# Performance work log

Hardware: AMD Instinct MI355X
Metric: run time of the kernel (lower is better)

The kernel has to match this reference:

```python
import jax, jax.numpy as jnp
import numpy as np
import math

EMBED_DIM = 256
NUM_HEADS = 8
FFN_DIM = 1024
EPS = 1e-5


def layer_norm(x, g, b):
    mu = jnp.mean(x, axis=-1, keepdims=True)
    var = jnp.var(x, axis=-1, keepdims=True)
    return (x - mu) / jnp.sqrt(var + EPS) * g + b


def setup_inputs() -> dict:
    key = jax.random.key(0)
    ks = jax.random.split(key, 10)
    B, L, D, F = 4, 2048, EMBED_DIM, FFN_DIM
    x = jax.random.normal(ks[0], (B, L, D), dtype=jnp.float32)
    mask = jnp.ones((B, L), dtype=jnp.int32)
    # FFN params (PyTorch Linear default-ish scale)
    W1 = jax.random.normal(ks[1], (D, F), dtype=jnp.float32) / np.sqrt(D)
    b1 = jnp.zeros((F,), dtype=jnp.float32)
    W2 = jax.random.normal(ks[2], (F, D), dtype=jnp.float32) / np.sqrt(F)
    b2 = jnp.zeros((D,), dtype=jnp.float32)
    g1 = jnp.ones((D,), dtype=jnp.float32)
    be1 = jnp.zeros((D,), dtype=jnp.float32)
    g2 = jnp.ones((D,), dtype=jnp.float32)
    be2 = jnp.zeros((D,), dtype=jnp.float32)
    return {"x": x, "mask": mask, "W1": W1, "b1": b1, "W2": W2, "b2": b2,
            "g1": g1, "be1": be1, "g2": g2, "be2": be2}


def quantum_attention(x, mask):
    B, L, D = x.shape
    H, dk = NUM_HEADS, D // NUM_HEADS
    xh = x.reshape(B, L, H, dk).transpose(0, 2, 1, 3)  # [B,H,L,dk]
    # per-token mean over batch and heads -> [L, dk]
    m = jnp.mean(xh, axis=(0, 1))
    # closed form of the single-qubit RX circuit: P(|1>) = sin^2(angle/2)
    dot = m @ m.T  # [L, L]
    ang = jnp.clip(dot, -math.pi, math.pi)
    scores = jnp.sin(ang * 0.5) ** 2  # [L, L], shared across B and H
    attn = jnp.broadcast_to(scores[None, None], (B, H, L, L))
    attn = jnp.where(mask[:, None, None, :] == 0, -1e9, attn)
    attn = jax.nn.softmax(attn, axis=-1)
    out = jnp.einsum('bhij,bhjd->bhid', attn, xh)  # values are xh itself
    return out.transpose(0, 2, 1, 3).reshape(B, L, D)


def reference(x, mask, W1, b1, W2, b2, g1, be1, g2, be2):
    attn_out = quantum_attention(x, mask)
    h = layer_norm(x + attn_out, g1, be1)
    ffn = jax.nn.relu(h @ W1 + b1) @ W2 + b2
    return layer_norm(h + ffn, g2, be2)
```

## Files before the change

### kernel.cpp

```cpp
#include <hip/hip_runtime.h>
#include <hip/hip_bf16.h>


#define B_ 4
#define L_ 2048
#define D_ 256
#define F_ 1024
#define PI_F 3.14159265358979323846f

typedef __bf16 bf16x8 __attribute__((ext_vector_type(8)));
typedef float floatx4 __attribute__((ext_vector_type(4)));
typedef unsigned short ushortx4 __attribute__((ext_vector_type(4)));

#define WAIT_VM(n) asm volatile("s_waitcnt vmcnt(" #n ")" ::: "memory")
#define SCHED0() __builtin_amdgcn_sched_barrier(0)
#define BARRIER() do { SCHED0(); __builtin_amdgcn_s_barrier(); SCHED0(); } while (0)

__device__ __forceinline__ unsigned short f2bf(float f) {
    unsigned int u = __float_as_uint(f);
    u = (u + 0x7FFFu + ((u >> 16) & 1u)) >> 16;
    return (unsigned short)u;
}
__device__ __forceinline__ float bf2f(unsigned short u) {
    union { unsigned int i; float f; } v; v.i = ((unsigned int)u) << 16; return v.f;
}

__device__ __forceinline__ void async_cp16(unsigned short* lds, const unsigned short* g) {
    __builtin_amdgcn_global_load_lds(
        (const __attribute__((address_space(1))) unsigned int*)g,
        (__attribute__((address_space(3))) unsigned int*)lds, 16, 0, 0);
}

__global__ __launch_bounds__(256) void k_prep(const float* __restrict__ x,
                                              const float* __restrict__ W1,
                                              const float* __restrict__ W2,
                                              const int* __restrict__ mask,
                                              unsigned short* __restrict__ mb,
                                              unsigned short* __restrict__ XmT,
                                              unsigned short* __restrict__ W1T,
                                              unsigned short* __restrict__ W2T) {
    __shared__ float tile[32][33];
    int r = blockIdx.x, t = threadIdx.x;
    if (r >= 2560) {
        if (r < 2816) {
            int idx = (r - 2560) * 256 + t;
            int l = idx >> 5, k = idx & 31;
            float s = 0.f;
#pragma unroll
            for (int b = 0; b < B_; b++) {
                const float* xp = x + ((size_t)(b * L_ + l)) * D_ + k;
#pragma unroll
                for (int h = 0; h < 8; h++) s += xp[h * 32];
            }
            mb[idx] = f2bf(s * (1.f / 32.f));
        } else {
#pragma unroll
            for (int c = 0; c < 32; c++) {
                int e = c * 256 + t;
                int b = e >> 11, j = e & (L_ - 1);
                XmT[(size_t)(1024 + b) * L_ + j] = mask[b * L_ + j] ? 0x3F80 : 0;
            }
        }
        return;
    }
    const float* in; unsigned short* outp; int R, C; const int* mrow = nullptr; size_t bo = 0;
    int bx, by;
    if (r < 2048) {
        int z = r >> 9, rem = r & 511; by = rem >> 3; bx = rem & 7;
        in = x; outp = XmT; R = L_; C = 256; bo = (size_t)z * R * C; mrow = mask + z * L_;
    } else if (r < 2304) {
        int rem = r - 2048; bx = rem & 31; by = rem >> 5;
        in = W1; outp = W1T; R = 256; C = 1024;
    } else {
        int rem = r - 2304; bx = rem & 7; by = rem >> 3;
        in = W2; outp = W2T; R = 1024; C = 256;
    }
    int r0 = by * 32, c0 = bx * 32;
    int tx = t & 31, ty = t >> 5;
#pragma unroll
    for (int rr = 0; rr < 4; rr++) {
        int rw = ty + rr * 8;
        tile[rw][tx] = in[bo + (size_t)(r0 + rw) * C + c0 + tx];
    }
    float mfac = 1.f;
    if (mrow) mfac = mrow[r0 + tx] ? 1.f : 0.f;
    __syncthreads();
#pragma unroll
    for (int rr = 0; rr < 4; rr++) {
        int c = ty + rr * 8;
        outp[bo + (size_t)(c0 + c) * R + r0 + tx] = f2bf(tile[tx][c] * mfac);
    }
}

__global__ __launch_bounds__(256) void k_scores_mfma(const unsigned short* __restrict__ mb,
                                                     unsigned short* __restrict__ E) {
    const int t = threadIdx.x, lane = t & 63, wid = t >> 6;
    const int wm = (wid >> 1) * 64, wn = (wid & 1) * 32;
    const int lr = lane & 15, lq = lane >> 4;
    int m0 = blockIdx.y * 128, n0 = blockIdx.x * 64;
    bf16x8 af[4], bfr[2];
#pragma unroll
    for (int i = 0; i < 4; i++)
        af[i] = *(const bf16x8*)(mb + (size_t)(m0 + wm + i * 16 + lr) * 32 + lq * 8);
#pragma unroll
    for (int j = 0; j < 2; j++)
        bfr[j] = *(const bf16x8*)(mb + (size_t)(n0 + wn + j * 16 + lr) * 32 + lq * 8);
    floatx4 acc[4][2];
#pragma unroll
    for (int i = 0; i < 4; i++)
#pragma unroll
        for (int j = 0; j < 2; j++) {
            acc[i][j] = (floatx4){0.f, 0.f, 0.f, 0.f};
            acc[i][j] = __builtin_amdgcn_mfma_f32_16x16x32_bf16(af[i], bfr[j], acc[i][j], 0, 0, 0);
        }
#pragma unroll
    for (int i = 0; i < 4; i++)
#pragma unroll
        for (int j = 0; j < 2; j++)
#pragma unroll
            for (int r = 0; r < 4; r++) {
                int row = m0 + wm + i * 16 + lq * 4 + r;
                int col = n0 + wn + j * 16 + lr;
                float d = fminf(fmaxf(acc[i][j][r], -PI_F), PI_F);
                float sn = __sinf(0.5f * d);
                E[(size_t)row * L_ + col] = f2bf(__expf(sn * sn));
            }
}

__global__ __launch_bounds__(256) void k_av(const unsigned short* __restrict__ E,
                                            const unsigned short* __restrict__ XmT,
                                            unsigned short* __restrict__ Cb) {
    __shared__ __align__(16) unsigned short sbuf[3][128 * 64 + 64 * 64];
    const int t = threadIdx.x, lane = t & 63, wid = t >> 6;
    const int wm = (wid >> 1) * 64, wn = (wid & 1) * 32;
    const int lr = lane & 15, lq = lane >> 4;
    const int lrow = lane >> 3, lseg = lane & 7;

    int bid = blockIdx.x;
    int swz = (bid & 7) * 34 + (bid >> 3);
    int m0 = (swz / 17) * 128, n0 = (swz % 17) * 64;

    const unsigned short* Ag[4]; int sAoff[4];
#pragma unroll
    for (int q = 0; q < 4; q++) {
        int rl = wid * 32 + q * 8 + lrow;
        Ag[q] = E + (size_t)(m0 + rl) * L_ + ((lseg - rl) & 7) * 8;
        sAoff[q] = (wid * 32 + q * 8) * 64;
    }
    const unsigned short* Bg[2]; int sBoff[2];
#pragma unroll
    for (int q = 0; q < 2; q++) {
        int rl = wid * 16 + q * 8 + lrow;
        Bg[q] = XmT + (size_t)(n0 + rl) * L_ + ((lseg - rl) & 7) * 8;
        sBoff[q] = 8192 + (wid * 16 + q * 8) * 64;
    }
    int arot[4], aroff[4], brot[2], broff[2];
#pragma unroll
    for (int i = 0; i < 4; i++) { int ar = wm + i * 16 + lr; aroff[i] = ar * 64; arot[i] = lq + ar; }
#pragma unroll
    for (int j = 0; j < 2; j++) { int br = wn + j * 16 + lr; broff[j] = 8192 + br * 64; brot[j] = lq + br; }

    floatx4 acc[4][2];
#pragma unroll
    for (int i = 0; i < 4; i++)
#pragma unroll
        for (int j = 0; j < 2; j++) acc[i][j] = (floatx4){0.f, 0.f, 0.f, 0.f};

    auto stage = [&](unsigned short* base, int k0) {
#pragma unroll
        for (int q = 0; q < 4; q++) async_cp16(base + sAoff[q], Ag[q] + k0);
#pragma unroll
        for (int q = 0; q < 2; q++) async_cp16(base + sBoff[q], Bg[q] + k0);
    };
    auto compute = [&](const unsigned short* base) {
#pragma unroll
        for (int s = 0; s < 2; s++) {
            bf16x8 af[4], bfr[2];
#pragma unroll
            for (int i = 0; i < 4; i++)
                af[i] = *(const bf16x8*)(base + aroff[i] + ((s * 4 + arot[i]) & 7) * 8);
#pragma unroll
            for (int j = 0; j < 2; j++)
                bfr[j] = *(const bf16x8*)(base + broff[j] + ((s * 4 + brot[j]) & 7) * 8);
#pragma unroll
            for (int i = 0; i < 4; i++)
#pragma unroll
                for (int j = 0; j < 2; j++)
                    acc[i][j] = __builtin_amdgcn_mfma_f32_16x16x32_bf16(af[i], bfr[j], acc[i][j], 0, 0, 0);
        }
    };

    unsigned short *p0 = sbuf[0], *p1 = sbuf[1], *p2 = sbuf[2];
    stage(p0, 0); stage(p1, 64); stage(p2, 128);
    WAIT_VM(12); BARRIER();
    for (int p = 0; p < 29; ++p) {
        compute(p0);
        BARRIER();
        stage(p0, (p + 3) << 6);
        WAIT_VM(12); BARRIER();
        unsigned short* tmp = p0; p0 = p1; p1 = p2; p2 = tmp;
    }
    compute(p0);
    BARRIER();
    WAIT_VM(6); BARRIER();
    compute(p1);
    BARRIER();
    WAIT_VM(0); BARRIER();
    compute(p2);

#pragma unroll
    for (int i = 0; i < 4; i++)
#pragma unroll
        for (int j = 0; j < 2; j++)
#pragma unroll
            for (int r = 0; r < 4; r++) {
                int row = m0 + wm + i * 16 + lq * 4 + r;
                int col = n0 + wn + j * 16 + lr;
                Cb[(size_t)row * 1088 + col] = f2bf(acc[i][j][r]);
            }
}

__global__ __launch_bounds__(256) void k_ln1(const float* __restrict__ x, const unsigned short* __restrict__ Cb,
                                             const float* __restrict__ g_, const float* __restrict__ be_,
                                             unsigned short* __restrict__ hb) {
    int t = threadIdx.x, wid = t >> 6, lane = t & 63;
    int tok = (blockIdx.x << 2) + wid;
    int b = tok >> 11, i = tok & (L_ - 1);
    float rs = bf2f(Cb[(size_t)i * 1088 + 1024 + b]);
    float4 xv = *(const float4*)(x + (size_t)tok * D_ + lane * 4);
    ushortx4 cv = *(const ushortx4*)(Cb + (size_t)i * 1088 + b * 256 + lane * 4);
    float v0 = xv.x + bf2f(cv.x) / rs;
    float v1 = xv.y + bf2f(cv.y) / rs;
    float v2 = xv.z + bf2f(cv.z) / rs;
    float v3 = xv.w + bf2f(cv.w) / rs;
    float s  = v0 + v1 + v2 + v3;
    float s2 = v0 * v0 + v1 * v1 + v2 * v2 + v3 * v3;
#pragma unroll
    for (int o = 1; o < 64; o <<= 1) { s += __shfl_xor(s, o); s2 += __shfl_xor(s2, o); }
    float mu = s * (1.f / 256.f);
    float var = s2 * (1.f / 256.f) - mu * mu;
    float r = rsqrtf(var + 1e-5f);
    float4 gv = *(const float4*)(g_ + lane * 4);
    float4 bv = *(const float4*)(be_ + lane * 4);
    ushortx4 o4;
    o4.x = f2bf((v0 - mu) * r * gv.x + bv.x);
    o4.y = f2bf((v1 - mu) * r * gv.y + bv.y);
    o4.z = f2bf((v2 - mu) * r * gv.z + bv.z);
    o4.w = f2bf((v3 - mu) * r * gv.w + bv.w);
    *(ushortx4*)(hb + (size_t)tok * D_ + lane * 4) = o4;
}

__global__ __launch_bounds__(256) void k_gemm1(const unsigned short* __restrict__ hb,
                                               const unsigned short* __restrict__ W1T,
                                               const float* __restrict__ b1, unsigned short* __restrict__ t1) {
    __shared__ __align__(16) unsigned short sbuf[2][128 * 64 + 128 * 64];
    const int t = threadIdx.x, lane = t & 63, wid = t >> 6;
    const int wm = (wid >> 1) * 64, wn = (wid & 1) * 64;
    const int lr = lane & 15, lq = lane >> 4;
    const int lrow8 = lane >> 3, lseg = lane & 7;

    int bid = blockIdx.x;
    int swz = (bid & 7) * 64 + (bid >> 3);
    int m0 = (swz >> 3) * 128, n0 = (swz & 7) * 128;

    const unsigned short* Ag[4]; const unsigned short* Bg[4]; int aoff[4], boff4[4];
#pragma unroll
    for (int q = 0; q < 4; q++) {
        int rl = q * 32 + wid * 8 + lrow8;
        int seg = (lseg - rl) & 7;
        Ag[q] = hb + (size_t)(m0 + rl) * 256 + seg * 8;
        Bg[q] = W1T + (size_t)(n0 + rl) * 256 + seg * 8;
        aoff[q] = (q * 32 + wid * 8) * 64;
        boff4[q] = 8192 + (q * 32 + wid * 8) * 64;
    }
    int arot[4], aroff[4], brot[4], broff[4];
#pragma unroll
    for (int i = 0; i < 4; i++) { int ar = wm + i * 16 + lr; aroff[i] = ar * 64; arot[i] = lq + ar; }
#pragma unroll
    for (int j = 0; j < 4; j++) { int br = wn + j * 16 + lr; broff[j] = 8192 + br * 64; brot[j] = lq + br; }

    floatx4 acc[4][4];
#pragma unroll
    for (int i = 0; i < 4; i++)
#pragma unroll
        for (int j = 0; j < 4; j++) acc[i][j] = (floatx4){0.f, 0.f, 0.f, 0.f};

    auto stage = [&](unsigned short* base, int k0) {
#pragma unroll
        for (int q = 0; q < 4; q++) { async_cp16(base + aoff[q], Ag[q] + k0); async_cp16(base + boff4[q], Bg[q] + k0); }
    };
    auto compute = [&](const unsigned short* base) {
#pragma unroll
        for (int s = 0; s < 2; s++) {
            bf16x8 af[4], bfr[4];
#pragma unroll
            for (int i = 0; i < 4; i++) af[i] = *(const bf16x8*)(base + aroff[i] + ((s * 4 + arot[i]) & 7) * 8);
#pragma unroll
            for (int j = 0; j < 4; j++) bfr[j] = *(const bf16x8*)(base + broff[j] + ((s * 4 + brot[j]) & 7) * 8);
#pragma unroll
            for (int i = 0; i < 4; i++)
#pragma unroll
                for (int j = 0; j < 4; j++)
                    acc[i][j] = __builtin_amdgcn_mfma_f32_16x16x32_bf16(af[i], bfr[j], acc[i][j], 0, 0, 0);
        }
    };

    unsigned short *pa = sbuf[0], *pb = sbuf[1];
    stage(pa, 0); stage(pb, 64);
    WAIT_VM(8); BARRIER();
    compute(pa);
    BARRIER();
    stage(pa, 128);
    WAIT_VM(8); BARRIER();
    compute(pb);
    BARRIER();
    stage(pb, 192);
    WAIT_VM(8); BARRIER();
    compute(pa);
    BARRIER();
    WAIT_VM(0); BARRIER();
    compute(pb);

    float bb[4];
#pragma unroll
    for (int j = 0; j < 4; j++) bb[j] = b1[n0 + wn + j * 16 + lr];
#pragma unroll
    for (int i = 0; i < 4; i++)
#pragma unroll
        for (int j = 0; j < 4; j++) {
            int col = n0 + wn + j * 16 + lr;
#pragma unroll
            for (int r = 0; r < 4; r++) {
                int row = m0 + wm + i * 16 + lq * 4 + r;
                t1[(size_t)row * 1024 + col] = f2bf(fmaxf(acc[i][j][r] + bb[j], 0.f));
            }
        }
}

__global__ __launch_bounds__(256) void k_gemm2ln(const unsigned short* __restrict__ t1,
                                                 const unsigned short* __restrict__ W2T,
                                                 const float* __restrict__ b2,
                                                 const unsigned short* __restrict__ hb,
                                                 const float* __restrict__ g_, const float* __restrict__ be_,
                                                 float* __restrict__ out) {
    __shared__ __align__(16) unsigned short sbuf[3][32 * 64 + 256 * 64];
    __shared__ float red[4][32][2];
    const int t = threadIdx.x, lane = t & 63, wid = t >> 6;
    const int wn = wid * 64;
    const int lr = lane & 15, lq = lane >> 4;
    const int lrow8 = lane >> 3, lseg = lane & 7;
    int m0 = blockIdx.x * 32;

    int arl = wid * 8 + lrow8;
    const unsigned short* Ag = t1 + (size_t)(m0 + arl) * 1024 + (((lseg - arl) & 7) * 8);
    int sAoff = (wid * 8) * 64;
    const unsigned short* Bg[8]; int sBoff[8];
#pragma unroll
    for (int q = 0; q < 8; q++) {
        int rl = q * 32 + wid * 8 + lrow8;
        Bg[q] = W2T + (size_t)rl * 1024 + (((lseg - rl) & 7) * 8);
        sBoff[q] = 2048 + (q * 32 + wid * 8) * 64;
    }
    int aroff[2], arot[2];
#pragma unroll
    for (int i = 0; i < 2; i++) { int ar = i * 16 + lr; aroff[i] = ar * 64; arot[i] = lq + ar; }
    int brot[4], broff[4];
#pragma unroll
    for (int j = 0; j < 4; j++) { int br = wn + j * 16 + lr; broff[j] = 2048 + br * 64; brot[j] = lq + br; }

    floatx4 acc[2][4];
#pragma unroll
    for (int i = 0; i < 2; i++)
#pragma unroll
        for (int j = 0; j < 4; j++) acc[i][j] = (floatx4){0.f, 0.f, 0.f, 0.f};

    auto stage = [&](unsigned short* base, int k0) {
        async_cp16(base + sAoff, Ag + k0);
#pragma unroll
        for (int q = 0; q < 8; q++) async_cp16(base + sBoff[q], Bg[q] + k0);
    };
    auto compute = [&](const unsigned short* base) {
#pragma unroll
        for (int s = 0; s < 2; s++) {
            bf16x8 af[2];
#pragma unroll
            for (int i = 0; i < 2; i++)
                af[i] = *(const bf16x8*)(base + aroff[i] + ((s * 4 + arot[i]) & 7) * 8);
#pragma unroll
            for (int j = 0; j < 4; j++) {
                bf16x8 bfr = *(const bf16x8*)(base + broff[j] + ((s * 4 + brot[j]) & 7) * 8);
#pragma unroll
                for (int i = 0; i < 2; i++)
                    acc[i][j] = __builtin_amdgcn_mfma_f32_16x16x32_bf16(af[i], bfr, acc[i][j], 0, 0, 0);
            }
        }
    };

    unsigned short *p0 = sbuf[0], *p1 = sbuf[1], *p2 = sbuf[2];
    stage(p0, 0); stage(p1, 64); stage(p2, 128);
    WAIT_VM(18); BARRIER();
    for (int p = 0; p < 13; ++p) {
        compute(p0);
        BARRIER();
        stage(p0, (p + 3) << 6);
        WAIT_VM(18); BARRIER();
        unsigned short* tmp = p0; p0 = p1; p1 = p2; p2 = tmp;
    }
    compute(p0);
    BARRIER();
    WAIT_VM(9); BARRIER();
    compute(p1);
    BARRIER();
    WAIT_VM(0); BARRIER();
    compute(p2);

    float psum[2][4], psq[2][4];
#pragma unroll
    for (int i = 0; i < 2; i++)
#pragma unroll
        for (int r = 0; r < 4; r++) { psum[i][r] = 0.f; psq[i][r] = 0.f; }
#pragma unroll
    for (int i = 0; i < 2; i++)
#pragma unroll
        for (int j = 0; j < 4; j++) {
            int col = wn + j * 16 + lr;
            float bv = b2[col];
#pragma unroll
            for (int r = 0; r < 4; r++) {
                int row = m0 + i * 16 + lq * 4 + r;
                float v = acc[i][j][r] + bv + bf2f(hb[(size_t)row * 256 + col]);
                acc[i][j][r] = v;
                psum[i][r] += v; psq[i][r] += v * v;
            }
        }
#pragma unroll
    for (int o = 1; o < 16; o <<= 1)
#pragma unroll
        for (int i = 0; i < 2; i++)
#pragma unroll
            for (int r = 0; r < 4; r++) { psum[i][r] += __shfl_xor(psum[i][r], o); psq[i][r] += __shfl_xor(psq[i][r], o); }
    if (lr == 0) {
#pragma unroll
        for (int i = 0; i < 2; i++)
#pragma unroll
            for (int r = 0; r < 4; r++) {
                int lrow = i * 16 + lq * 4 + r;
                red[wid][lrow][0] = psum[i][r];
                red[wid][lrow][1] = psq[i][r];
            }
    }
    __syncthreads();
#pragma unroll
    for (int i = 0; i < 2; i++)
#pragma unroll
        for (int r = 0; r < 4; r++) {
            int lrow = i * 16 + lq * 4 + r;
            float s  = red[0][lrow][0] + red[1][lrow][0] + red[2][lrow][0] + red[3][lrow][0];
            float s2 = red[0][lrow][1] + red[1][lrow][1] + red[2][lrow][1] + red[3][lrow][1];
            float mu = s * (1.f / 256.f);
            float var = s2 * (1.f / 256.f) - mu * mu;
            float rc = rsqrtf(var + 1e-5f);
            int row = m0 + lrow;
#pragma unroll
            for (int j = 0; j < 4; j++) {
                int col = wn + j * 16 + lr;
                out[(size_t)row * 256 + col] = (acc[i][j][r] - mu) * rc * g_[col] + be_[col];
            }
        }
}

extern "C" void kernel_launch(void* const* d_in, const int* in_sizes, int n_in,
                              void* d_out, int out_size, void* d_ws, size_t ws_size,
                              hipStream_t stream) {
    const float* x   = (const float*)d_in[0];
    const int*  mask = (const int*)d_in[1];
    const float* W1  = (const float*)d_in[2];
    const float* b1  = (const float*)d_in[3];
    const float* W2  = (const float*)d_in[4];
    const float* b2  = (const float*)d_in[5];
    const float* g1  = (const float*)d_in[6];
    const float* be1 = (const float*)d_in[7];
    const float* g2  = (const float*)d_in[8];
    const float* be2 = (const float*)d_in[9];
    float* out = (float*)d_out;

    char* w = (char*)d_ws;
    unsigned short* mb_   = (unsigned short*)w;  w += 65536 * 2;
    unsigned short* E_    = (unsigned short*)w;  w += (size_t)L_ * L_ * 2;
    unsigned short* XmT_  = (unsigned short*)w;  w += (size_t)1088 * L_ * 2;
    unsigned short* W1T_  = (unsigned short*)w;  w += 262144 * 2;
    unsigned short* W2T_  = (unsigned short*)w;  w += 262144 * 2;
    unsigned short* Cb_   = (unsigned short*)w;  w += (size_t)L_ * 1088 * 2;
    unsigned short* hb_   = (unsigned short*)w;  w += (size_t)8192 * 256 * 2;
    unsigned short* t1_   = (unsigned short*)w;  w += (size_t)8192 * 1024 * 2;

    k_prep<<<2817, 256, 0, stream>>>(x, W1, W2, mask, mb_, XmT_, W1T_, W2T_);
    k_scores_mfma<<<dim3(32, 16), 256, 0, stream>>>(mb_, E_);
    k_av<<<272, 256, 0, stream>>>(E_, XmT_, Cb_);
    k_ln1<<<2048, 256, 0, stream>>>(x, Cb_, g1, be1, hb_);
    k_gemm1<<<512, 256, 0, stream>>>(hb_, W1T_, b1, t1_);
    k_gemm2ln<<<256, 256, 0, stream>>>(t1_, W2T_, b2, hb_, g2, be2, out);
}
```

Baseline: 137.5 us.

## Fuse LN1, FFN GEMM1 and GEMM2+LN2 into a single streaming kernel

Replaces the three kernels (LN1, GEMM1, GEMM2+LN2) with one fused kernel. Each block of 32 tokens computes LN1 into LDS, then loops over 64-wide FFN chunks: GEMM1 chunk, bias+ReLU into an LDS tile, and an immediate GEMM2 accumulate. W1/W2 chunks are double-buffered with async loads, and the residual is read back from LDS. This removes the global round-trips of the hb and t1 intermediates and two launches. The cost is only 256 blocks at one block per CU, many barriers per chunk, and GEMM1 recomputed with small tiles, so latency hiding may suffer.

```diff
diff --git a/kernel.cpp b/kernel.cpp
--- a/kernel.cpp
+++ b/kernel.cpp
@@ -11,8 +11,10 @@
 typedef __bf16 bf16x8 __attribute__((ext_vector_type(8)));
 typedef float floatx4 __attribute__((ext_vector_type(4)));
 typedef unsigned short ushortx4 __attribute__((ext_vector_type(4)));
+typedef unsigned short ushortx8 __attribute__((ext_vector_type(8)));
 
 #define WAIT_VM(n) asm volatile("s_waitcnt vmcnt(" #n ")" ::: "memory")
+#define WAIT_LGKM() asm volatile("s_waitcnt lgkmcnt(0)" ::: "memory")
 #define SCHED0() __builtin_amdgcn_sched_barrier(0)
 #define BARRIER() do { SCHED0(); __builtin_amdgcn_s_barrier(); SCHED0(); } while (0)
 
@@ -220,215 +222,195 @@
             }
 }
 
-__global__ __launch_bounds__(256) void k_ln1(const float* __restrict__ x, const unsigned short* __restrict__ Cb,
-                                             const float* __restrict__ g_, const float* __restrict__ be_,
-                                             unsigned short* __restrict__ hb) {
-    int t = threadIdx.x, wid = t >> 6, lane = t & 63;
-    int tok = (blockIdx.x << 2) + wid;
-    int b = tok >> 11, i = tok & (L_ - 1);
-    float rs = bf2f(Cb[(size_t)i * 1088 + 1024 + b]);
-    float4 xv = *(const float4*)(x + (size_t)tok * D_ + lane * 4);
-    ushortx4 cv = *(const ushortx4*)(Cb + (size_t)i * 1088 + b * 256 + lane * 4);
-    float v0 = xv.x + bf2f(cv.x) / rs;
-    float v1 = xv.y + bf2f(cv.y) / rs;
-    float v2 = xv.z + bf2f(cv.z) / rs;
-    float v3 = xv.w + bf2f(cv.w) / rs;
-    float s  = v0 + v1 + v2 + v3;
-    float s2 = v0 * v0 + v1 * v1 + v2 * v2 + v3 * v3;
-#pragma unroll
-    for (int o = 1; o < 64; o <<= 1) { s += __shfl_xor(s, o); s2 += __shfl_xor(s2, o); }
-    float mu = s * (1.f / 256.f);
-    float var = s2 * (1.f / 256.f) - mu * mu;
-    float r = rsqrtf(var + 1e-5f);
-    float4 gv = *(const float4*)(g_ + lane * 4);
-    float4 bv = *(const float4*)(be_ + lane * 4);
-    ushortx4 o4;
-    o4.x = f2bf((v0 - mu) * r * gv.x + bv.x);
-    o4.y = f2bf((v1 - mu) * r * gv.y + bv.y);
-    o4.z = f2bf((v2 - mu) * r * gv.z + bv.z);
-    o4.w = f2bf((v3 - mu) * r * gv.w + bv.w);
-    *(ushortx4*)(hb + (size_t)tok * D_ + lane * 4) = o4;
-}
-
-__global__ __launch_bounds__(256) void k_gemm1(const unsigned short* __restrict__ hb,
-                                               const unsigned short* __restrict__ W1T,
-                                               const float* __restrict__ b1, unsigned short* __restrict__ t1) {
-    __shared__ __align__(16) unsigned short sbuf[2][128 * 64 + 128 * 64];
+__global__ __launch_bounds__(256, 1) void k_ffn(const float* __restrict__ x,
+                                                const unsigned short* __restrict__ Cb,
+                                                const unsigned short* __restrict__ W1T,
+                                                const unsigned short* __restrict__ W2T,
+                                                const float* __restrict__ b1,
+                                                const float* __restrict__ b2,
+                                                const float* __restrict__ g1, const float* __restrict__ be1,
+                                                const float* __restrict__ g2, const float* __restrict__ be2,
+                                                float* __restrict__ out) {
+    __shared__ __align__(16) unsigned short hA[4 * 32 * 64];
+    __shared__ __align__(16) unsigned short W1b[2][4 * 64 * 64];
+    __shared__ __align__(16) unsigned short W2b[4 * 64 * 64];
+    __shared__ __align__(16) unsigned short t1c[32 * 72];
+    __shared__ float red[4][32][2];
+
     const int t = threadIdx.x, lane = t & 63, wid = t >> 6;
-    const int wm = (wid >> 1) * 64, wn = (wid & 1) * 64;
     const int lr = lane & 15, lq = lane >> 4;
-    const int lrow8 = lane >> 3, lseg = lane & 7;
-
-    int bid = blockIdx.x;
-    int swz = (bid & 7) * 64 + (bid >> 3);
-    int m0 = (swz >> 3) * 128, n0 = (swz & 7) * 128;
-
-    const unsigned short* Ag[4]; const unsigned short* Bg[4]; int aoff[4], boff4[4];
-#pragma unroll
-    for (int q = 0; q < 4; q++) {
-        int rl = q * 32 + wid * 8 + lrow8;
-        int seg = (lseg - rl) & 7;
-        Ag[q] = hb + (size_t)(m0 + rl) * 256 + seg * 8;
-        Bg[q] = W1T + (size_t)(n0 + rl) * 256 + seg * 8;
-        aoff[q] = (q * 32 + wid * 8) * 64;
-        boff4[q] = 8192 + (q * 32 + wid * 8) * 64;
-    }
-    int arot[4], aroff[4], brot[4], broff[4];
-#pragma unroll
-    for (int i = 0; i < 4; i++) { int ar = wm + i * 16 + lr; aroff[i] = ar * 64; arot[i] = lq + ar; }
-#pragma unroll
-    for (int j = 0; j < 4; j++) { int br = wn + j * 16 + lr; broff[j] = 8192 + br * 64; brot[j] = lq + br; }
-
-    floatx4 acc[4][4];
-#pragma unroll
-    for (int i = 0; i < 4; i++)
+    const int half = lane >> 5, l32 = lane & 31;
+    const int m0 = blockIdx.x * 32;
+
+    float b1v[16];
+#pragma unroll
+    for (int c = 0; c < 16; c++) b1v[c] = b1[c * 64 + wid * 16 + lr];
+    float4 g1a = *(const float4*)(g1 + l32 * 8);
+    float4 g1b = *(const float4*)(g1 + l32 * 8 + 4);
+    float4 be1a = *(const float4*)(be1 + l32 * 8);
+    float4 be1b = *(const float4*)(be1 + l32 * 8 + 4);
+    WAIT_VM(0);
+
+    auto stageW1 = [&](unsigned short* buf, int fc) {
+#pragma unroll
+        for (int q = 0; q < 8; q++) {
+            int kc = q >> 1, sub = q & 1;
+            int fl = sub * 32 + wid * 8 + (lane >> 3);
+            int kk = lane & 7;
+            const unsigned short* src = W1T + (size_t)(fc * 64 + fl) * 256 + kc * 64 + (((kk - fl) & 7) * 8);
+            async_cp16(W1b[0] + (buf - W1b[0]) + kc * 4096 + sub * 2048 + wid * 512, src);
+        }
+    };
+    auto stageW2 = [&](int fc) {
+#pragma unroll
+        for (int q = 0; q < 8; q++) {
+            int nc = q >> 1, sub = q & 1;
+            int nl = sub * 32 + wid * 8 + (lane >> 3);
+            int kk = lane & 7;
+            const unsigned short* src = W2T + (size_t)(nc * 64 + nl) * 1024 + fc * 64 + (((kk - nl) & 7) * 8);
+            async_cp16(W2b + nc * 4096 + sub * 2048 + wid * 512, src);
+        }
+    };
+    stageW1(W1b[0], 0);
+    stageW2(0);
+    stageW1(W1b[1], 1);
+
+#pragma unroll
+    for (int it = 0; it < 4; it++) {
+        int tloc = wid * 8 + it * 2 + half;
+        int tok = m0 + tloc;
+        int bi = tok >> 11, ii = tok & (L_ - 1);
+        float rs = bf2f(Cb[(size_t)ii * 1088 + 1024 + bi]);
+        float4 xv0 = *(const float4*)(x + (size_t)tok * D_ + l32 * 8);
+        float4 xv1 = *(const float4*)(x + (size_t)tok * D_ + l32 * 8 + 4);
+        ushortx8 cv = *(const ushortx8*)(Cb + (size_t)ii * 1088 + bi * 256 + l32 * 8);
+        float v[8];
+        v[0] = xv0.x + bf2f(cv[0]) / rs; v[1] = xv0.y + bf2f(cv[1]) / rs;
+        v[2] = xv0.z + bf2f(cv[2]) / rs; v[3] = xv0.w + bf2f(cv[3]) / rs;
+        v[4] = xv1.x + bf2f(cv[4]) / rs; v[5] = xv1.y + bf2f(cv[5]) / rs;
+        v[6] = xv1.z + bf2f(cv[6]) / rs; v[7] = xv1.w + bf2f(cv[7]) / rs;
+        float s = 0.f, s2 = 0.f;
+#pragma unroll
+        for (int k = 0; k < 8; k++) { s += v[k]; s2 += v[k] * v[k]; }
+#pragma unroll
+        for (int o = 1; o < 32; o <<= 1) { s += __shfl_xor(s, o); s2 += __shfl_xor(s2, o); }
+        float mu = s * (1.f / 256.f);
+        float var = s2 * (1.f / 256.f) - mu * mu;
+        float rq = rsqrtf(var + 1e-5f);
+        union { bf16x8 v8; unsigned short u[8]; } hv;
+        hv.u[0] = f2bf((v[0] - mu) * rq * g1a.x + be1a.x);
+        hv.u[1] = f2bf((v[1] - mu) * rq * g1a.y + be1a.y);
+        hv.u[2] = f2bf((v[2] - mu) * rq * g1a.z + be1a.z);
+        hv.u[3] = f2bf((v[3] - mu) * rq * g1a.w + be1a.w);
+        hv.u[4] = f2bf((v[4] - mu) * rq * g1b.x + be1b.x);
+        hv.u[5] = f2bf((v[5] - mu) * rq * g1b.y + be1b.y);
+        hv.u[6] = f2bf((v[6] - mu) * rq * g1b.z + be1b.z);
+        hv.u[7] = f2bf((v[7] - mu) * rq * g1b.w + be1b.w);
+        *(bf16x8*)(hA + (l32 >> 3) * 2048 + tloc * 64 + ((((l32 & 7) + tloc) & 7) * 8)) = hv.v8;
+    }
+    WAIT_LGKM(); BARRIER();
+
+    bf16x8 haf[2][8];
+#pragma unroll
+    for (int i = 0; i < 2; i++)
+#pragma unroll
+        for (int kc = 0; kc < 4; kc++)
+#pragma unroll
+            for (int s = 0; s < 2; s++) {
+                int row = i * 16 + lr;
+                haf[i][kc * 2 + s] = *(const bf16x8*)(hA + kc * 2048 + row * 64 + (((s * 4 + lq + row) & 7) * 8));
+            }
+
+    floatx4 acc[2][4];
+#pragma unroll
+    for (int i = 0; i < 2; i++)
 #pragma unroll
         for (int j = 0; j < 4; j++) acc[i][j] = (floatx4){0.f, 0.f, 0.f, 0.f};
 
-    auto stage = [&](unsigned short* base, int k0) {
-#pragma unroll
-        for (int q = 0; q < 4; q++) { async_cp16(base + aoff[q], Ag[q] + k0); async_cp16(base + boff4[q], Bg[q] + k0); }
-    };
-    auto compute = [&](const unsigned short* base) {
+    const int wcol = wid * 16 + lr;
+    auto gemm1 = [&](const unsigned short* wb, floatx4 a1[2]) {
+#pragma unroll
+        for (int kc = 0; kc < 4; kc++)
+#pragma unroll
+            for (int s = 0; s < 2; s++) {
+                bf16x8 bfr = *(const bf16x8*)(wb + kc * 4096 + wcol * 64 + (((s * 4 + lq + wcol) & 7) * 8));
+                a1[0] = __builtin_amdgcn_mfma_f32_16x16x32_bf16(haf[0][kc * 2 + s], bfr, a1[0], 0, 0, 0);
+                a1[1] = __builtin_amdgcn_mfma_f32_16x16x32_bf16(haf[1][kc * 2 + s], bfr, a1[1], 0, 0, 0);
+            }
+    };
+    auto t1write = [&](floatx4 a1[2], float bv) {
+#pragma unroll
+        for (int i = 0; i < 2; i++)
+#pragma unroll
+            for (int r = 0; r < 4; r++)
+                t1c[(i * 16 + lq * 4 + r) * 72 + wcol] = f2bf(fmaxf(a1[i][r] + bv, 0.f));
+    };
+    auto gemm2 = [&]() {
 #pragma unroll
         for (int s = 0; s < 2; s++) {
-            bf16x8 af[4], bfr[4];
-#pragma unroll
-            for (int i = 0; i < 4; i++) af[i] = *(const bf16x8*)(base + aroff[i] + ((s * 4 + arot[i]) & 7) * 8);
-#pragma unroll
-            for (int j = 0; j < 4; j++) bfr[j] = *(const bf16x8*)(base + broff[j] + ((s * 4 + brot[j]) & 7) * 8);
-#pragma unroll
-            for (int i = 0; i < 4; i++)
-#pragma unroll
-                for (int j = 0; j < 4; j++)
-                    acc[i][j] = __builtin_amdgcn_mfma_f32_16x16x32_bf16(af[i], bfr[j], acc[i][j], 0, 0, 0);
-        }
-    };
-
-    unsigned short *pa = sbuf[0], *pb = sbuf[1];
-    stage(pa, 0); stage(pb, 64);
-    WAIT_VM(8); BARRIER();
-    compute(pa);
-    BARRIER();
-    stage(pa, 128);
-    WAIT_VM(8); BARRIER();
-    compute(pb);
-    BARRIER();
-    stage(pb, 192);
-    WAIT_VM(8); BARRIER();
-    compute(pa);
-    BARRIER();
-    WAIT_VM(0); BARRIER();
-    compute(pb);
-
-    float bb[4];
-#pragma unroll
-    for (int j = 0; j < 4; j++) bb[j] = b1[n0 + wn + j * 16 + lr];
-#pragma unroll
-    for (int i = 0; i < 4; i++)
+            bf16x8 af0 = *(const bf16x8*)(t1c + lr * 72 + s * 32 + lq * 8);
+            bf16x8 af1 = *(const bf16x8*)(t1c + (16 + lr) * 72 + s * 32 + lq * 8);
+#pragma unroll
+            for (int j = 0; j < 4; j++) {
+                int nl = j * 16 + lr;
+                bf16x8 bfr = *(const bf16x8*)(W2b + wid * 4096 + nl * 64 + (((s * 4 + lq + nl) & 7) * 8));
+                acc[0][j] = __builtin_amdgcn_mfma_f32_16x16x32_bf16(af0, bfr, acc[0][j], 0, 0, 0);
+                acc[1][j] = __builtin_amdgcn_mfma_f32_16x16x32_bf16(af1, bfr, acc[1][j], 0, 0, 0);
+            }
+        }
+    };
+
+#pragma unroll
+    for (int c = 0; c < 14; c++) {
+        floatx4 a1[2] = { (floatx4){0.f,0.f,0.f,0.f}, (floatx4){0.f,0.f,0.f,0.f} };
+        gemm1(W1b[c & 1], a1);
+        BARRIER();
+        stageW1(W1b[c & 1], c + 2);
+        t1write(a1, b1v[c]);
+        WAIT_LGKM();
+        WAIT_VM(8); BARRIER();
+        gemm2();
+        BARRIER();
+        stageW2(c + 1);
+    }
+    {
+        floatx4 a1[2] = { (floatx4){0.f,0.f,0.f,0.f}, (floatx4){0.f,0.f,0.f,0.f} };
+        gemm1(W1b[0], a1);
+        BARRIER();
+        t1write(a1, b1v[14]);
+        WAIT_LGKM();
+        WAIT_VM(0); BARRIER();
+        gemm2();
+        BARRIER();
+        stageW2(15);
+    }
+    {
+        floatx4 a1[2] = { (floatx4){0.f,0.f,0.f,0.f}, (floatx4){0.f,0.f,0.f,0.f} };
+        gemm1(W1b[1], a1);
+        BARRIER();
+        t1write(a1, b1v[15]);
+        WAIT_LGKM();
+        WAIT_VM(0); BARRIER();
+        gemm2();
+    }
+
+    float psum[2][4], psq[2][4];
+#pragma unroll
+    for (int i = 0; i < 2; i++)
+#pragma unroll
+        for (int r = 0; r < 4; r++) { psum[i][r] = 0.f; psq[i][r] = 0.f; }
+#pragma unroll
+    for (int i = 0; i < 2; i++)
 #pragma unroll
         for (int j = 0; j < 4; j++) {
-            int col = n0 + wn + j * 16 + lr;
+            int col = wid * 64 + j * 16 + lr;
+            float bv = b2[col];
+            int kc = col >> 6, ks = (col >> 3) & 7, ke = col & 7;
 #pragma unroll
             for (int r = 0; r < 4; r++) {
-                int row = m0 + wm + i * 16 + lq * 4 + r;
-                t1[(size_t)row * 1024 + col] = f2bf(fmaxf(acc[i][j][r] + bb[j], 0.f));
-            }
-        }
-}
-
-__global__ __launch_bounds__(256) void k_gemm2ln(const unsigned short* __restrict__ t1,
-                                                 const unsigned short* __restrict__ W2T,
-                                                 const float* __restrict__ b2,
-                                                 const unsigned short* __restrict__ hb,
-                                                 const float* __restrict__ g_, const float* __restrict__ be_,
-                                                 float* __restrict__ out) {
-    __shared__ __align__(16) unsigned short sbuf[3][32 * 64 + 256 * 64];
-    __shared__ float red[4][32][2];
-    const int t = threadIdx.x, lane = t & 63, wid = t >> 6;
-    const int wn = wid * 64;
-    const int lr = lane & 15, lq = lane >> 4;
-    const int lrow8 = lane >> 3, lseg = lane & 7;
-    int m0 = blockIdx.x * 32;
-
-    int arl = wid * 8 + lrow8;
-    const unsigned short* Ag = t1 + (size_t)(m0 + arl) * 1024 + (((lseg - arl) & 7) * 8);
-    int sAoff = (wid * 8) * 64;
-    const unsigned short* Bg[8]; int sBoff[8];
-#pragma unroll
-    for (int q = 0; q < 8; q++) {
-        int rl = q * 32 + wid * 8 + lrow8;
-        Bg[q] = W2T + (size_t)rl * 1024 + (((lseg - rl) & 7) * 8);
-        sBoff[q] = 2048 + (q * 32 + wid * 8) * 64;
-    }
-    int aroff[2], arot[2];
-#pragma unroll
-    for (int i = 0; i < 2; i++) { int ar = i * 16 + lr; aroff[i] = ar * 64; arot[i] = lq + ar; }
-    int brot[4], broff[4];
-#pragma unroll
-    for (int j = 0; j < 4; j++) { int br = wn + j * 16 + lr; broff[j] = 2048 + br * 64; brot[j] = lq + br; }
-
-    floatx4 acc[2][4];
-#pragma unroll
-    for (int i = 0; i < 2; i++)
-#pragma unroll
-        for (int j = 0; j < 4; j++) acc[i][j] = (floatx4){0.f, 0.f, 0.f, 0.f};
-
-    auto stage = [&](unsigned short* base, int k0) {
-        async_cp16(base + sAoff, Ag + k0);
-#pragma unroll
-        for (int q = 0; q < 8; q++) async_cp16(base + sBoff[q], Bg[q] + k0);
-    };
-    auto compute = [&](const unsigned short* base) {
-#pragma unroll
-        for (int s = 0; s < 2; s++) {
-            bf16x8 af[2];
-#pragma unroll
-            for (int i = 0; i < 2; i++)
-                af[i] = *(const bf16x8*)(base + aroff[i] + ((s * 4 + arot[i]) & 7) * 8);
-#pragma unroll
-            for (int j = 0; j < 4; j++) {
-                bf16x8 bfr = *(const bf16x8*)(base + broff[j] + ((s * 4 + brot[j]) & 7) * 8);
-#pragma unroll
-                for (int i = 0; i < 2; i++)
-                    acc[i][j] = __builtin_amdgcn_mfma_f32_16x16x32_bf16(af[i], bfr, acc[i][j], 0, 0, 0);
-            }
-        }
-    };
-
-    unsigned short *p0 = sbuf[0], *p1 = sbuf[1], *p2 = sbuf[2];
-    stage(p0, 0); stage(p1, 64); stage(p2, 128);
-    WAIT_VM(18); BARRIER();
-    for (int p = 0; p < 13; ++p) {
-        compute(p0);
-        BARRIER();
-        stage(p0, (p + 3) << 6);
-        WAIT_VM(18); BARRIER();
-        unsigned short* tmp = p0; p0 = p1; p1 = p2; p2 = tmp;
-    }
-    compute(p0);
-    BARRIER();
-    WAIT_VM(9); BARRIER();
-    compute(p1);
-    BARRIER();
-    WAIT_VM(0); BARRIER();
-    compute(p2);
-
-    float psum[2][4], psq[2][4];
-#pragma unroll
-    for (int i = 0; i < 2; i++)
-#pragma unroll
-        for (int r = 0; r < 4; r++) { psum[i][r] = 0.f; psq[i][r] = 0.f; }
-#pragma unroll
-    for (int i = 0; i < 2; i++)
-#pragma unroll
-        for (int j = 0; j < 4; j++) {
-            int col = wn + j * 16 + lr;
-            float bv = b2[col];
-#pragma unroll
-            for (int r = 0; r < 4; r++) {
-                int row = m0 + i * 16 + lq * 4 + r;
-                float v = acc[i][j][r] + bv + bf2f(hb[(size_t)row * 256 + col]);
+                int row = i * 16 + lq * 4 + r;
+                float hres = bf2f(hA[kc * 2048 + row * 64 + (((ks + row) & 7) * 8) + ke]);
+                float v = acc[i][j][r] + bv + hres;
                 acc[i][j][r] = v;
                 psum[i][r] += v; psq[i][r] += v * v;
             }
@@ -463,8 +445,8 @@
             int row = m0 + lrow;
 #pragma unroll
             for (int j = 0; j < 4; j++) {
-                int col = wn + j * 16 + lr;
-                out[(size_t)row * 256 + col] = (acc[i][j][r] - mu) * rc * g_[col] + be_[col];
+                int col = wid * 64 + j * 16 + lr;
+                out[(size_t)row * 256 + col] = (acc[i][j][r] - mu) * rc * g2[col] + be2[col];
             }
         }
 }
@@ -491,13 +473,9 @@
     unsigned short* W1T_  = (unsigned short*)w;  w += 262144 * 2;
     unsigned short* W2T_  = (unsigned short*)w;  w += 262144 * 2;
     unsigned short* Cb_   = (unsigned short*)w;  w += (size_t)L_ * 1088 * 2;
-    unsigned short* hb_   = (unsigned short*)w;  w += (size_t)8192 * 256 * 2;
-    unsigned short* t1_   = (unsigned short*)w;  w += (size_t)8192 * 1024 * 2;
 
     k_prep<<<2817, 256, 0, stream>>>(x, W1, W2, mask, mb_, XmT_, W1T_, W2T_);
     k_scores_mfma<<<dim3(32, 16), 256, 0, stream>>>(mb_, E_);
     k_av<<<272, 256, 0, stream>>>(E_, XmT_, Cb_);
-    k_ln1<<<2048, 256, 0, stream>>>(x, Cb_, g1, be1, hb_);
-    k_gemm1<<<512, 256, 0, stream>>>(hb_, W1T_, b1, t1_);
-    k_gemm2ln<<<256, 256, 0, stream>>>(t1_, W2T_, b2, hb_, g2, be2, out);
-}
+    k_ffn<<<256, 256, 0, stream>>>(x, Cb_, W1T_, W2T_, b1, b2, g1, be1, g2, be2, out);
+}
```

New measurement: 134.0 us. 1.03x faster.
